# Kernel optimization log

Measured on AMD Instinct MI355X. Metric: run time of the kernel, lower is better.

## Reference

```python
import jax, jax.numpy as jnp
import numpy as np

B = 64; FEAT = 16; T = 32001; BANDS = 8; ND = 16
OUT_LEN = 32000; N_TAPS = 43; K_LATE = 1024
FLIP_PROB = 0.1  # 1 - stickiness (0.9)


def _dense(k, fan_in, fan_out, scale=1.0):
    return jax.random.normal(k, (fan_in, fan_out), jnp.float32) * (scale / np.sqrt(fan_in))


def setup_inputs() -> dict:
    key = jax.random.key(0)
    ks = jax.random.split(key, 20)
    z32 = lambda n: jnp.zeros((n,), jnp.float32)
    inp = {}
    inp['x'] = jax.random.normal(ks[0], (B, FEAT), jnp.float32)
    # stand-in LSTM decoder params: (B, FEAT) -> (B, T, BANDS)
    inp['lstm_W1'] = _dense(ks[1], FEAT, 64); inp['lstm_b1'] = z32(64)
    inp['lstm_W2'] = _dense(ks[2], 64, T * BANDS); inp['lstm_b2'] = z32(T * BANDS)
    # EDCToFDNMapper params
    inp['enc_W1'] = _dense(ks[3], 2 * BANDS, 64); inp['enc_b1'] = z32(64)
    inp['enc_W2'] = _dense(ks[4], 64, 64); inp['enc_b2'] = z32(64)
    inp['del_W1'] = _dense(ks[5], 3 + 64, 64); inp['del_b1'] = z32(64)
    inp['del_W2'] = _dense(ks[6], 64, ND); inp['del_b2'] = z32(ND)
    inp['alp_W1'] = _dense(ks[7], 64, 32); inp['alp_b1'] = z32(32)
    inp['alp_W2'] = _dense(ks[8], 32, ND); inp['alp_b2'] = z32(ND)
    inp['bet_W1'] = _dense(ks[9], 64, 32); inp['bet_b1'] = z32(32)
    inp['bet_W2'] = _dense(ks[10], 32, ND); inp['bet_b2'] = z32(ND)
    # EarlyReflections gains (nn.Parameter, zeros-init in torch; random here to exercise math)
    inp['early_gains'] = jax.random.normal(ks[11], (N_TAPS,), jnp.float32) * 0.1
    # DifferentiableFDN surrogate: causal decaying FIR reverb kernel
    decay = jnp.exp(-jnp.arange(K_LATE, dtype=jnp.float32) / 256.0)
    inp['late_kernel'] = jax.random.normal(ks[12], (K_LATE,), jnp.float32) * 0.05 * decay
    # sticky-sign flip events (constant random draws, flip prob = 1 - stickiness)
    inp['flips'] = (jax.random.uniform(ks[13], (B, OUT_LEN)) < FLIP_PROB).astype(jnp.int32)
    return inp


def _causal_conv(sig, gains):
    # torch: F.conv1d(x[:,None,:], gains.flip(0)[None,None,:], padding=K-1)[:, 0, :L]
    # (torch conv1d is correlation; flipping makes it true convolution with gains)
    K = gains.shape[0]
    y = jax.lax.conv_general_dilated(sig[:, None, :], gains[::-1][None, None, :], (1,),
                                     [(K - 1, K - 1)], dimension_numbers=('NCH', 'OIH', 'NCH'))
    return y[:, 0, :sig.shape[1]]


def _mlp2(h, W1, b1, W2, b2):  # Linear-ReLU-Linear
    return jax.nn.relu(h @ W1 + b1) @ W2 + b2


def reference(x, lstm_W1, lstm_b1, lstm_W2, lstm_b2,
              enc_W1, enc_b1, enc_W2, enc_b2,
              del_W1, del_b1, del_W2, del_b2,
              alp_W1, alp_b1, alp_W2, alp_b2,
              bet_W1, bet_b1, bet_W2, bet_b2,
              early_gains, late_kernel, flips):
    Bx = x.shape[0]
    # LSTM stand-in: (B, FEAT) -> (B, T, BANDS)
    edc_pred = _mlp2(x, lstm_W1, lstm_b1, lstm_W2, lstm_b2).reshape(Bx, T, BANDS)
    edc_1d = edc_pred.mean(axis=2)  # (B, T)
    # EDCToFDNMapper
    edc_mean = edc_pred.mean(axis=1)
    q1 = edc_pred[:, :T // 4, :].mean(axis=1)
    q4 = edc_pred[:, 3 * T // 4:, :].mean(axis=1)
    edc_feat = jnp.concatenate([edc_mean, q4 - q1], axis=1)  # (B, 2*BANDS)
    h = jax.nn.relu(_mlp2(edc_feat, enc_W1, enc_b1, enc_W2, enc_b2))  # Linear-ReLU-Linear-ReLU
    delay_in = jnp.concatenate([x[:, :3], h], axis=1)
    log_kappa = _mlp2(delay_in, del_W1, del_b1, del_W2, del_b2)
    alpha_raw = _mlp2(h, alp_W1, alp_b1, alp_W2, alp_b2)
    beta_raw = _mlp2(h, bet_W1, bet_b1, bet_W2, bet_b2)
    # late reverb (FDN surrogate) + early reflections, both causal convs on edc_1d
    late = _causal_conv(edc_1d, late_kernel)[:, :OUT_LEN]   # (B, 32000)
    early = _causal_conv(edc_1d, early_gains)[:, :OUT_LEN]  # (B, 32000)
    # sign-sticky phase reconstruction: signs = (-1)^cumsum(flips[:,1:]) (parallel parity scan)
    diff = edc_1d[:, :-1] - edc_1d[:, 1:]
    amp = jnp.sqrt(jnp.clip(diff, 0.0))  # (B, T-1) == (B, 32000)
    par = jnp.cumsum(flips.at[:, 0].set(0), axis=1) % 2  # loop starts at t=1; signs[:,0]=+1
    phase = amp * (1.0 - 2.0 * par.astype(amp.dtype))
    rir = (early + late) * phase
    return (rir, edc_pred, log_kappa, alpha_raw, beta_raw)
```

## Files before the change

### kernel.cpp

```cpp
#include <hip/hip_runtime.h>
#include <hip/hip_bf16.h>

#define LJ 256008
#define TN 32001
#define OUT_LEN 32000

typedef __attribute__((ext_vector_type(8))) short short8v;
typedef __attribute__((ext_vector_type(8))) __bf16 bf16x8;
typedef __attribute__((ext_vector_type(4))) float f32x4;

__device__ __forceinline__ unsigned short f2bu(float f) {
    union { __hip_bfloat16 h; unsigned short u; } cv; cv.h = __float2bfloat16(f); return cv.u;
}

__global__ __launch_bounds__(256) void k_h1(const float* __restrict__ x,
                                            const float* __restrict__ W1,
                                            const float* __restrict__ b1,
                                            float* __restrict__ h1)
{
    int idx = blockIdx.x * 256 + threadIdx.x;
    if (idx >= 4096) return;
    int b = idx >> 6, i = idx & 63;
    float acc = b1[i];
    #pragma unroll
    for (int f = 0; f < 16; ++f)
        acc += x[b * 16 + f] * W1[f * 64 + i];
    h1[i * 64 + b] = fmaxf(acc, 0.f);
}

__global__ __launch_bounds__(512, 4) void k_gemm(const float* __restrict__ W2,
                                                 const float* __restrict__ b2,
                                                 const float* __restrict__ h1,
                                                 float* __restrict__ edc,
                                                 float* __restrict__ edc1d,
                                                 float* __restrict__ P)
{
    __shared__ float h1s[4096];
    int tid = threadIdx.x;
    for (int r = tid; r < 4096; r += 512) h1s[r] = h1[r];
    __syncthreads();
    int lane = tid & 63, wv = tid >> 6;
    int bstart = wv * 8;
    long jb4 = (long)blockIdx.x * 256 + 4 * lane;
    bool ok = jb4 < LJ;
    float acc[8][4];
    #pragma unroll
    for (int b = 0; b < 8; ++b)
        #pragma unroll
        for (int c = 0; c < 4; ++c) acc[b][c] = 0.f;
    for (int i = 0; i < 64; ++i) {
        float4 w = ok ? *(const float4*)(W2 + (long)i * LJ + jb4)
                      : make_float4(0.f, 0.f, 0.f, 0.f);
        const float4* hv = (const float4*)(h1s + i * 64 + bstart);
        #pragma unroll
        for (int b4 = 0; b4 < 2; ++b4) {
            float4 h4 = hv[b4];
            acc[b4*4+0][0] += h4.x * w.x; acc[b4*4+0][1] += h4.x * w.y;
            acc[b4*4+0][2] += h4.x * w.z; acc[b4*4+0][3] += h4.x * w.w;
            acc[b4*4+1][0] += h4.y * w.x; acc[b4*4+1][1] += h4.y * w.y;
            acc[b4*4+1][2] += h4.y * w.z; acc[b4*4+1][3] += h4.y * w.w;
            acc[b4*4+2][0] += h4.z * w.x; acc[b4*4+2][1] += h4.z * w.y;
            acc[b4*4+2][2] += h4.z * w.z; acc[b4*4+2][3] += h4.z * w.w;
            acc[b4*4+3][0] += h4.w * w.x; acc[b4*4+3][1] += h4.w * w.y;
            acc[b4*4+3][2] += h4.w * w.z; acc[b4*4+3][3] += h4.w * w.w;
        }
    }
    float4 bias = ok ? *(const float4*)(b2 + jb4) : make_float4(0.f, 0.f, 0.f, 0.f);
    int tcol = (int)(jb4 >> 3);
    #pragma unroll
    for (int b = 0; b < 8; ++b) {
        int bb = bstart + b;
        float r0, r1, r2, r3;
        if (ok) {
            float4 v = make_float4(acc[b][0] + bias.x, acc[b][1] + bias.y,
                                   acc[b][2] + bias.z, acc[b][3] + bias.w);
            *(float4*)(edc + (long)bb * LJ + jb4) = v;
            float s = v.x + v.y + v.z + v.w;
            s += __shfl_xor(s, 1);
            if ((lane & 1) == 0)
                edc1d[(long)bb * TN + tcol] = s * 0.125f;
            r0 = v.x; r1 = v.y; r2 = v.z; r3 = v.w;
        } else { r0 = r1 = r2 = r3 = 0.f; }
        r0 += __shfl_xor(r0, 2);  r1 += __shfl_xor(r1, 2);
        r2 += __shfl_xor(r2, 2);  r3 += __shfl_xor(r3, 2);
        r0 += __shfl_xor(r0, 4);  r1 += __shfl_xor(r1, 4);
        r2 += __shfl_xor(r2, 4);  r3 += __shfl_xor(r3, 4);
        r0 += __shfl_xor(r0, 8);  r1 += __shfl_xor(r1, 8);
        r2 += __shfl_xor(r2, 8);  r3 += __shfl_xor(r3, 8);
        r0 += __shfl_xor(r0, 16); r1 += __shfl_xor(r1, 16);
        r2 += __shfl_xor(r2, 16); r3 += __shfl_xor(r3, 16);
        r0 += __shfl_xor(r0, 32); r1 += __shfl_xor(r1, 32);
        r2 += __shfl_xor(r2, 32); r3 += __shfl_xor(r3, 32);
        if (lane < 2)
            *(float4*)(P + (long)blockIdx.x * 512 + bb * 8 + lane * 4)
                = make_float4(r0, r1, r2, r3);
    }
}

__global__ __launch_bounds__(512) void k_redsum(const float* __restrict__ P,
                                                float* __restrict__ sums)
{
    int g = blockIdx.x, t = threadIdx.x;
    int b = t >> 3, band = t & 7;
    int s0 = g * 16, s1 = s0 + 16;
    if (s1 > 1001) s1 = 1001;
    float all = 0.f, q1 = 0.f, q4 = 0.f;
    for (int blk = s0; blk < s1; ++blk) {
        float v = P[(long)blk * 512 + t];
        all += v;
        if (blk < 250) q1 += v;
        if (blk >= 750) q4 += v;
    }
    atomicAdd(&sums[b * 24 + band * 3 + 0], all);
    atomicAdd(&sums[b * 24 + band * 3 + 1], q1);
    atomicAdd(&sums[b * 24 + band * 3 + 2], q4);
}

__global__ __launch_bounds__(64) void k_mlp(const float* __restrict__ x,
    const float* __restrict__ sums,
    const float* __restrict__ eW1, const float* __restrict__ eb1,
    const float* __restrict__ eW2, const float* __restrict__ eb2,
    const float* __restrict__ dW1, const float* __restrict__ db1,
    const float* __restrict__ dW2, const float* __restrict__ db2,
    const float* __restrict__ aW1, const float* __restrict__ ab1,
    const float* __restrict__ aW2, const float* __restrict__ ab2,
    const float* __restrict__ bW1, const float* __restrict__ bb1,
    const float* __restrict__ bW2, const float* __restrict__ bb2,
    float* __restrict__ out_lk, float* __restrict__ out_a, float* __restrict__ out_b)
{
    int b = blockIdx.x, o = threadIdx.x;
    __shared__ float feat[16], a1[64], hh[64], t1[64];
    if (o < 16) {
        float v;
        if (o < 8) v = sums[b * 24 + o * 3] * (1.f / 32001.f);
        else {
            int band = o - 8;
            v = sums[b * 24 + band * 3 + 2] * (1.f / 8001.f)
              - sums[b * 24 + band * 3 + 1] * (1.f / 8000.f);
        }
        feat[o] = v;
    }
    __syncthreads();
    {   float acc = eb1[o];
        #pragma unroll
        for (int c = 0; c < 16; ++c) acc += feat[c] * eW1[c * 64 + o];
        a1[o] = fmaxf(acc, 0.f); }
    __syncthreads();
    {   float acc = eb2[o];
        for (int c = 0; c < 64; ++c) acc += a1[c] * eW2[c * 64 + o];
        hh[o] = fmaxf(acc, 0.f); }
    __syncthreads();
    {   float acc = db1[o];
        #pragma unroll
        for (int c = 0; c < 3; ++c) acc += x[b * 16 + c] * dW1[c * 64 + o];
        for (int c = 0; c < 64; ++c) acc += hh[c] * dW1[(3 + c) * 64 + o];
        t1[o] = fmaxf(acc, 0.f); }
    __syncthreads();
    if (o < 16) {
        float acc = db2[o];
        for (int c = 0; c < 64; ++c) acc += t1[c] * dW2[c * 16 + o];
        out_lk[b * 16 + o] = acc;
    }
    __syncthreads();
    if (o < 32) {
        float acc = ab1[o];
        for (int c = 0; c < 64; ++c) acc += hh[c] * aW1[c * 32 + o];
        t1[o] = fmaxf(acc, 0.f);
    }
    __syncthreads();
    if (o < 16) {
        float acc = ab2[o];
        for (int c = 0; c < 32; ++c) acc += t1[c] * aW2[c * 16 + o];
        out_a[b * 16 + o] = acc;
    }
    __syncthreads();
    if (o < 32) {
        float acc = bb1[o];
        for (int c = 0; c < 64; ++c) acc += hh[c] * bW1[c * 32 + o];
        t1[o] = fmaxf(acc, 0.f);
    }
    __syncthreads();
    if (o < 16) {
        float acc = bb2[o];
        for (int c = 0; c < 32; ++c) acc += t1[c] * bW2[c * 16 + o];
        out_b[b * 16 + o] = acc;
    }
}

__global__ __launch_bounds__(256) void k_par1(const int* __restrict__ flips,
                                              unsigned* __restrict__ parbits,
                                              unsigned* __restrict__ ctot)
{
    int b = blockIdx.x, c = blockIdx.y, tid = threadIdx.x;
    int t = c * 256 + tid;
    int bit = (t == 0) ? 0 : (flips[(long)b * OUT_LEN + t] & 1);
    int lane = tid & 63, wv = tid >> 6;
    unsigned long long mask = __ballot(bit != 0);
    int below = ((int)__popcll(mask & ((1ull << lane) - 1ull))) & 1;
    int incl = below ^ bit;
    __shared__ int wtot[4];
    if (lane == 0) wtot[wv] = ((int)__popcll(mask)) & 1;
    __syncthreads();
    int pre = 0;
    for (int w = 0; w < wv; ++w) pre ^= wtot[w];
    int inclB = pre ^ incl;
    unsigned long long m2 = __ballot(inclB != 0);
    if (lane == 0)  parbits[b * 1000 + c * 8 + wv * 2 + 0] = (unsigned)(m2 & 0xffffffffull);
    if (lane == 32) parbits[b * 1000 + c * 8 + wv * 2 + 1] = (unsigned)(m2 >> 32);
    if (tid == 0) ctot[c * 64 + b] = (unsigned)(wtot[0] ^ wtot[1] ^ wtot[2] ^ wtot[3]);
}

__global__ __launch_bounds__(64) void k_par2(const unsigned* __restrict__ ctot,
                                             unsigned* __restrict__ cpref)
{
    int b = threadIdx.x;
    unsigned carry = 0;
    for (int c = 0; c < 125; ++c) {
        cpref[c * 64 + b] = carry;
        carry ^= ctot[c * 64 + b];
    }
}

__global__ __launch_bounds__(512) void k_convm(const float* __restrict__ edc1d,
    const float* __restrict__ lk, const float* __restrict__ eg,
    const unsigned* __restrict__ parbits, const unsigned* __restrict__ cpref,
    float* __restrict__ rir)
{
    __shared__ float kerf[1024];
    __shared__ __align__(16) unsigned short afr[33 * 64 * 8];
    __shared__ __align__(16) unsigned short sbf[3136];
    __shared__ float sf32[2049];
    int b = blockIdx.x, tb0 = blockIdx.y * 2048, tid = threadIdx.x;
    const float* src = edc1d + (long)b * TN;
    for (int k = tid; k < 1024; k += 512)
        kerf[k] = lk[k] + (k < 43 ? eg[k] : 0.f);
    for (int ch = tid; ch < 388; ch += 512) {
        unsigned short h[8];
        #pragma unroll
        for (int e = 0; e < 8; ++e) {
            int gt = tb0 + ch * 8 + e - 1031;
            float v = (gt >= 0 && gt <= OUT_LEN) ? src[gt] : 0.f;
            h[e] = f2bu(v);
        }
        int cs = ch ^ ((ch >> 3) & 7);
        *(uint4*)(&sbf[cs * 8]) = make_uint4(
            (unsigned)h[0] | ((unsigned)h[1] << 16), (unsigned)h[2] | ((unsigned)h[3] << 16),
            (unsigned)h[4] | ((unsigned)h[5] << 16), (unsigned)h[6] | ((unsigned)h[7] << 16));
    }
    for (int u = tid; u < 2049; u += 512) {
        int gt = tb0 + u;
        sf32[u] = (gt <= OUT_LEN) ? src[gt] : 0.f;
    }
    __syncthreads();
    for (int sl = tid; sl < 33 * 64; sl += 512) {
        int kb = sl >> 6, l = sl & 63;
        int x0 = kb * 32 - 1 + (l & 15) - 8 * (l >> 4);
        unsigned short h[8];
        #pragma unroll
        for (int e = 0; e < 8; ++e) {
            int x = x0 - e;
            float v = (x >= 0 && x < 1024) ? kerf[x] : 0.f;
            h[e] = f2bu(v);
        }
        *(uint4*)(&afr[sl * 8]) = make_uint4(
            (unsigned)h[0] | ((unsigned)h[1] << 16), (unsigned)h[2] | ((unsigned)h[3] << 16),
            (unsigned)h[4] | ((unsigned)h[5] << 16), (unsigned)h[6] | ((unsigned)h[7] << 16));
    }
    __syncthreads();
    int lane = tid & 63, wv = tid >> 6;
    int tb = tb0 + wv * 256;
    int cq = wv * 256 + 16 * (lane & 15) + 8 * (lane >> 4) + 1032;
    f32x4 acc = {0.f, 0.f, 0.f, 0.f};
    for (int kb = 0; kb < 33; ++kb) {
        short8v araw = *(const short8v*)(&afr[(kb * 64 + lane) * 8]);
        int ch = (cq - (kb << 5)) >> 3;
        int cs = ch ^ ((ch >> 3) & 7);
        short8v braw = *(const short8v*)(&sbf[cs * 8]);
        union { short8v s; bf16x8 v; } ua, ub2;
        ua.s = araw; ub2.s = braw;
        acc = __builtin_amdgcn_mfma_f32_16x16x32_bf16(ua.v, ub2.v, acc, 0, 0, 0);
    }
    int c = lane & 15, q = lane >> 4;
    int t4 = tb + 16 * c + 4 * q;
    if (t4 < OUT_LEN) {
        int u0 = t4 - tb0;
        unsigned pw = parbits[b * 1000 + (t4 >> 5)];
        unsigned cp = cpref[(t4 >> 8) * 64 + b] & 1u;
        int sh = t4 & 31;
        float sv[5];
        #pragma unroll
        for (int e = 0; e < 5; ++e) sv[e] = sf32[u0 + e];
        float r[4];
        #pragma unroll
        for (int reg = 0; reg < 4; ++reg) {
            float diff = sv[reg] - sv[reg + 1];
            float amp = diff > 0.f ? sqrtf(diff) : 0.f;
            unsigned p = ((pw >> (sh + reg)) & 1u) ^ cp;
            r[reg] = acc[reg] * amp * (p ? -1.f : 1.f);
        }
        *(float4*)(rir + (long)b * OUT_LEN + t4) = make_float4(r[0], r[1], r[2], r[3]);
    }
}

extern "C" void kernel_launch(void* const* d_in, const int* in_sizes, int n_in,
                              void* d_out, int out_size, void* d_ws, size_t ws_size,
                              hipStream_t stream) {
    (void)in_sizes; (void)n_in; (void)out_size; (void)ws_size;
    const float* x    = (const float*)d_in[0];
    const float* lW1  = (const float*)d_in[1];  const float* lb1 = (const float*)d_in[2];
    const float* lW2  = (const float*)d_in[3];  const float* lb2 = (const float*)d_in[4];
    const float* eW1  = (const float*)d_in[5];  const float* eb1 = (const float*)d_in[6];
    const float* eW2  = (const float*)d_in[7];  const float* eb2 = (const float*)d_in[8];
    const float* dW1  = (const float*)d_in[9];  const float* db1 = (const float*)d_in[10];
    const float* dW2  = (const float*)d_in[11]; const float* db2 = (const float*)d_in[12];
    const float* aW1  = (const float*)d_in[13]; const float* ab1 = (const float*)d_in[14];
    const float* aW2  = (const float*)d_in[15]; const float* ab2 = (const float*)d_in[16];
    const float* bW1  = (const float*)d_in[17]; const float* bb1 = (const float*)d_in[18];
    const float* bW2  = (const float*)d_in[19]; const float* bb2 = (const float*)d_in[20];
    const float* eg   = (const float*)d_in[21]; const float* lkk = (const float*)d_in[22];
    const int* flips  = (const int*)d_in[23];

    float* out = (float*)d_out;
    float* rir = out;
    float* edc = out + 2048000;
    float* olk = out + 18432512;
    float* oa  = out + 18433536;
    float* ob  = out + 18434560;

    char* wsb = (char*)d_ws;
    float*    ws_h1   = (float*)(wsb + 1024);
    unsigned* ws_ct   = (unsigned*)(wsb + 18432);
    unsigned* ws_cp   = (unsigned*)(wsb + 50688);
    unsigned* ws_pb   = (unsigned*)(wsb + 82944);
    float*    ws_sums = (float*)(wsb + 339200);
    float*    ws_e1d  = (float*)(wsb + 346112);
    float*    ws_part = (float*)(wsb + 8538368);

    hipMemsetAsync(ws_sums, 0, 64 * 24 * sizeof(float), stream);

    k_h1<<<16, 256, 0, stream>>>(x, lW1, lb1, ws_h1);
    k_par1<<<dim3(64, 125), 256, 0, stream>>>(flips, ws_pb, ws_ct);
    k_par2<<<1, 64, 0, stream>>>(ws_ct, ws_cp);
    k_gemm<<<1001, 512, 0, stream>>>(lW2, lb2, ws_h1, edc, ws_e1d, ws_part);
    k_redsum<<<63, 512, 0, stream>>>(ws_part, ws_sums);
    k_mlp<<<64, 64, 0, stream>>>(x, ws_sums, eW1, eb1, eW2, eb2, dW1, db1, dW2, db2,
                                 aW1, ab1, aW2, ab2, bW1, bb1, bW2, bb2, olk, oa, ob);
    k_convm<<<dim3(64, 16), 512, 0, stream>>>(ws_e1d, lkk, eg, ws_pb, ws_cp, rir);
}
```

Before: 105.8 us.

## Stage W2 rows through double-buffered LDS shared across waves in GEMM

Previously each of the 8 waves in a block read the same 64 rows of W2 from global memory, one row per iteration. Now each wave loads one of 8 rows per chunk into a double-buffered shared-memory tile, and all waves read the weights from LDS while the next chunk is prefetched. This aims to cut redundant global/L2 traffic on the large W2 matrix and overlap loads with FMAs. In exchange it adds a barrier per chunk and more LDS use, and it drops the occupancy hint from the launch bounds.

```diff
diff --git a/kernel.cpp b/kernel.cpp
--- a/kernel.cpp
+++ b/kernel.cpp
@@ -28,44 +28,70 @@
     h1[i * 64 + b] = fmaxf(acc, 0.f);
 }
 
-__global__ __launch_bounds__(512, 4) void k_gemm(const float* __restrict__ W2,
-                                                 const float* __restrict__ b2,
-                                                 const float* __restrict__ h1,
-                                                 float* __restrict__ edc,
-                                                 float* __restrict__ edc1d,
-                                                 float* __restrict__ P)
+__global__ __launch_bounds__(512) void k_gemm(const float* __restrict__ W2,
+                                              const float* __restrict__ b2,
+                                              const float* __restrict__ h1,
+                                              float* __restrict__ edc,
+                                              float* __restrict__ edc1d,
+                                              float* __restrict__ P)
 {
     __shared__ float h1s[4096];
+    __shared__ float w2s[2][2048];
     int tid = threadIdx.x;
-    for (int r = tid; r < 4096; r += 512) h1s[r] = h1[r];
-    __syncthreads();
+    #pragma unroll
+    for (int r = 0; r < 8; ++r) h1s[tid + 512 * r] = h1[tid + 512 * r];
     int lane = tid & 63, wv = tid >> 6;
     int bstart = wv * 8;
     long jb4 = (long)blockIdx.x * 256 + 4 * lane;
     bool ok = jb4 < LJ;
+    const float* wb = W2 + (ok ? jb4 : 0);
+    int myslot = wv * 256 + 4 * lane;
     float acc[8][4];
     #pragma unroll
     for (int b = 0; b < 8; ++b)
         #pragma unroll
         for (int c = 0; c < 4; ++c) acc[b][c] = 0.f;
-    for (int i = 0; i < 64; ++i) {
-        float4 w = ok ? *(const float4*)(W2 + (long)i * LJ + jb4)
-                      : make_float4(0.f, 0.f, 0.f, 0.f);
-        const float4* hv = (const float4*)(h1s + i * 64 + bstart);
-        #pragma unroll
-        for (int b4 = 0; b4 < 2; ++b4) {
-            float4 h4 = hv[b4];
-            acc[b4*4+0][0] += h4.x * w.x; acc[b4*4+0][1] += h4.x * w.y;
-            acc[b4*4+0][2] += h4.x * w.z; acc[b4*4+0][3] += h4.x * w.w;
-            acc[b4*4+1][0] += h4.y * w.x; acc[b4*4+1][1] += h4.y * w.y;
-            acc[b4*4+1][2] += h4.y * w.z; acc[b4*4+1][3] += h4.y * w.w;
-            acc[b4*4+2][0] += h4.z * w.x; acc[b4*4+2][1] += h4.z * w.y;
-            acc[b4*4+2][2] += h4.z * w.z; acc[b4*4+2][3] += h4.z * w.w;
-            acc[b4*4+3][0] += h4.w * w.x; acc[b4*4+3][1] += h4.w * w.y;
-            acc[b4*4+3][2] += h4.w * w.z; acc[b4*4+3][3] += h4.w * w.w;
-        }
-    }
-    float4 bias = ok ? *(const float4*)(b2 + jb4) : make_float4(0.f, 0.f, 0.f, 0.f);
+
+    {
+        float4 v0 = *(const float4*)(wb + (long)wv * LJ);
+        *(float4*)(&w2s[0][myslot]) = v0;
+    }
+    __syncthreads();
+
+    #pragma unroll 1
+    for (int cc = 0; cc < 8; ++cc) {
+        int buf = cc & 1;
+        float4 vx;
+        bool more = (cc + 1) < 8;
+        if (more) vx = *(const float4*)(wb + (long)((cc + 1) * 8 + wv) * LJ);
+        #pragma unroll
+        for (int i = 0; i < 8; ++i) {
+            float4 w = *(const float4*)(&w2s[buf][i * 256 + 4 * lane]);
+            const float4* hv = (const float4*)(h1s + (cc * 8 + i) * 64 + bstart);
+            float4 ha = hv[0], hb = hv[1];
+            acc[0][0] += ha.x * w.x; acc[0][1] += ha.x * w.y;
+            acc[0][2] += ha.x * w.z; acc[0][3] += ha.x * w.w;
+            acc[1][0] += ha.y * w.x; acc[1][1] += ha.y * w.y;
+            acc[1][2] += ha.y * w.z; acc[1][3] += ha.y * w.w;
+            acc[2][0] += ha.z * w.x; acc[2][1] += ha.z * w.y;
+            acc[2][2] += ha.z * w.z; acc[2][3] += ha.z * w.w;
+            acc[3][0] += ha.w * w.x; acc[3][1] += ha.w * w.y;
+            acc[3][2] += ha.w * w.z; acc[3][3] += ha.w * w.w;
+            acc[4][0] += hb.x * w.x; acc[4][1] += hb.x * w.y;
+            acc[4][2] += hb.x * w.z; acc[4][3] += hb.x * w.w;
+            acc[5][0] += hb.y * w.x; acc[5][1] += hb.y * w.y;
+            acc[5][2] += hb.y * w.z; acc[5][3] += hb.y * w.w;
+            acc[6][0] += hb.z * w.x; acc[6][1] += hb.z * w.y;
+            acc[6][2] += hb.z * w.z; acc[6][3] += hb.z * w.w;
+            acc[7][0] += hb.w * w.x; acc[7][1] += hb.w * w.y;
+            acc[7][2] += hb.w * w.z; acc[7][3] += hb.w * w.w;
+        }
+        if (more) *(float4*)(&w2s[buf ^ 1][myslot]) = vx;
+        __syncthreads();
+    }
+
+    float4 z4 = make_float4(0.f, 0.f, 0.f, 0.f);
+    float4 bias = ok ? *(const float4*)(b2 + jb4) : z4;
     int tcol = (int)(jb4 >> 3);
     #pragma unroll
     for (int b = 0; b < 8; ++b) {
```

Result: slower. 116.2 us (+9.9%).

## Compute decoder output GEMM with bf16 MFMA and derive band means from band-summed weights

Applied to the files above, without the earlier changes.

Replaces the FP32 FMA outer-product GEMM that produces the decoder output with bf16 16x16x32 MFMA tiles staged through shared memory, in two K halves. The per-time-step band mean is computed separately in FP32 by pre-summing W2 and the bias over each group of eight columns and dotting with h1, so that value keeps full precision. The aim is to cut ALU work in the GEMM. In exchange, the edc output drops to bf16 input precision, and W2 is loaded with narrower strided accesses and read twice.

```diff
diff --git a/kernel.cpp b/kernel.cpp
--- a/kernel.cpp
+++ b/kernel.cpp
@@ -11,6 +11,17 @@
 
 __device__ __forceinline__ unsigned short f2bu(float f) {
     union { __hip_bfloat16 h; unsigned short u; } cv; cv.h = __float2bfloat16(f); return cv.u;
+}
+__device__ __forceinline__ uint4 pack8(const unsigned short* h) {
+    return make_uint4((unsigned)h[0] | ((unsigned)h[1] << 16),
+                      (unsigned)h[2] | ((unsigned)h[3] << 16),
+                      (unsigned)h[4] | ((unsigned)h[5] << 16),
+                      (unsigned)h[6] | ((unsigned)h[7] << 16));
+}
+__device__ __forceinline__ f32x4 mfma16(uint4 a, uint4 b, f32x4 c) {
+    union { uint4 u; short8v s; bf16x8 v; } ua, ub;
+    ua.u = a; ub.u = b;
+    return __builtin_amdgcn_mfma_f32_16x16x32_bf16(ua.v, ub.v, c, 0, 0, 0);
 }
 
 __global__ __launch_bounds__(256) void k_h1(const float* __restrict__ x,
@@ -28,72 +39,158 @@
     h1[i * 64 + b] = fmaxf(acc, 0.f);
 }
 
-__global__ __launch_bounds__(512, 4) void k_gemm(const float* __restrict__ W2,
-                                                 const float* __restrict__ b2,
-                                                 const float* __restrict__ h1,
-                                                 float* __restrict__ edc,
-                                                 float* __restrict__ edc1d,
-                                                 float* __restrict__ P)
-{
-    __shared__ float h1s[4096];
+__global__ __launch_bounds__(512) void k_gemm(const float* __restrict__ W2,
+                                              const float* __restrict__ b2,
+                                              const float* __restrict__ h1,
+                                              float* __restrict__ edc,
+                                              float* __restrict__ edc1d,
+                                              float* __restrict__ P)
+{
+    __shared__ float h1f[4096];
+    __shared__ __align__(16) unsigned short afr[4096];
+    __shared__ __align__(16) unsigned short bfr[8192];
+    __shared__ float wband[2048];
+    __shared__ float bband[32];
     int tid = threadIdx.x;
-    for (int r = tid; r < 4096; r += 512) h1s[r] = h1[r];
-    __syncthreads();
+    long C0 = (long)blockIdx.x * 256;
+
+    #pragma unroll
+    for (int s = 0; s < 8; ++s) h1f[tid + 512 * s] = h1[tid + 512 * s];
+    {
+        int bt = tid >> 7, kb = (tid >> 6) & 1, l = tid & 63;
+        int q = l >> 4, r = l & 15;
+        unsigned short hh[8];
+        #pragma unroll
+        for (int e = 0; e < 8; ++e)
+            hh[e] = f2bu(h1[(32 * kb + 8 * q + e) * 64 + 16 * bt + r]);
+        *(uint4*)(&afr[tid * 8]) = pack8(hh);
+    }
+    #pragma unroll
+    for (int s = 0; s < 4; ++s) {
+        int en = tid + 512 * s;
+        int i = en >> 5, tl = en & 31;
+        long c8 = C0 + 8 * tl;
+        float sum = 0.f;
+        if (c8 + 7 < LJ) {
+            float4 u0 = *(const float4*)(W2 + (long)i * LJ + c8);
+            float4 u1 = *(const float4*)(W2 + (long)i * LJ + c8 + 4);
+            sum = ((u0.x + u0.y) + (u0.z + u0.w)) + ((u1.x + u1.y) + (u1.z + u1.w));
+        }
+        wband[i * 32 + tl] = sum;
+    }
+    if (tid < 32) {
+        long c8 = C0 + 8 * tid;
+        float sum = 0.f;
+        if (c8 + 7 < LJ) {
+            float4 u0 = *(const float4*)(b2 + c8);
+            float4 u1 = *(const float4*)(b2 + c8 + 4);
+            sum = ((u0.x + u0.y) + (u0.z + u0.w)) + ((u1.x + u1.y) + (u1.z + u1.w));
+        }
+        bband[tid] = sum;
+    }
+    #pragma unroll
+    for (int s = 0; s < 2; ++s) {
+        int sl = tid + 512 * s;
+        int ct = sl >> 6, l = sl & 63;
+        int q = l >> 4, r = l & 15;
+        long col = C0 + 16 * ct + r;
+        unsigned short hh[8];
+        #pragma unroll
+        for (int e = 0; e < 8; ++e) {
+            float v = (col < LJ) ? W2[(long)(8 * q + e) * LJ + col] : 0.f;
+            hh[e] = f2bu(v);
+        }
+        *(uint4*)(&bfr[sl * 8]) = pack8(hh);
+    }
+    __syncthreads();
+
     int lane = tid & 63, wv = tid >> 6;
-    int bstart = wv * 8;
-    long jb4 = (long)blockIdx.x * 256 + 4 * lane;
-    bool ok = jb4 < LJ;
-    float acc[8][4];
-    #pragma unroll
-    for (int b = 0; b < 8; ++b)
-        #pragma unroll
-        for (int c = 0; c < 4; ++c) acc[b][c] = 0.f;
-    for (int i = 0; i < 64; ++i) {
-        float4 w = ok ? *(const float4*)(W2 + (long)i * LJ + jb4)
-                      : make_float4(0.f, 0.f, 0.f, 0.f);
-        const float4* hv = (const float4*)(h1s + i * 64 + bstart);
-        #pragma unroll
-        for (int b4 = 0; b4 < 2; ++b4) {
-            float4 h4 = hv[b4];
-            acc[b4*4+0][0] += h4.x * w.x; acc[b4*4+0][1] += h4.x * w.y;
-            acc[b4*4+0][2] += h4.x * w.z; acc[b4*4+0][3] += h4.x * w.w;
-            acc[b4*4+1][0] += h4.y * w.x; acc[b4*4+1][1] += h4.y * w.y;
-            acc[b4*4+1][2] += h4.y * w.z; acc[b4*4+1][3] += h4.y * w.w;
-            acc[b4*4+2][0] += h4.z * w.x; acc[b4*4+2][1] += h4.z * w.y;
-            acc[b4*4+2][2] += h4.z * w.z; acc[b4*4+2][3] += h4.z * w.w;
-            acc[b4*4+3][0] += h4.w * w.x; acc[b4*4+3][1] += h4.w * w.y;
-            acc[b4*4+3][2] += h4.w * w.z; acc[b4*4+3][3] += h4.w * w.w;
-        }
-    }
-    float4 bias = ok ? *(const float4*)(b2 + jb4) : make_float4(0.f, 0.f, 0.f, 0.f);
-    int tcol = (int)(jb4 >> 3);
-    #pragma unroll
-    for (int b = 0; b < 8; ++b) {
-        int bb = bstart + b;
-        float r0, r1, r2, r3;
-        if (ok) {
-            float4 v = make_float4(acc[b][0] + bias.x, acc[b][1] + bias.y,
-                                   acc[b][2] + bias.z, acc[b][3] + bias.w);
-            *(float4*)(edc + (long)bb * LJ + jb4) = v;
-            float s = v.x + v.y + v.z + v.w;
-            s += __shfl_xor(s, 1);
-            if ((lane & 1) == 0)
-                edc1d[(long)bb * TN + tcol] = s * 0.125f;
-            r0 = v.x; r1 = v.y; r2 = v.z; r3 = v.w;
-        } else { r0 = r1 = r2 = r3 = 0.f; }
-        r0 += __shfl_xor(r0, 2);  r1 += __shfl_xor(r1, 2);
-        r2 += __shfl_xor(r2, 2);  r3 += __shfl_xor(r3, 2);
-        r0 += __shfl_xor(r0, 4);  r1 += __shfl_xor(r1, 4);
-        r2 += __shfl_xor(r2, 4);  r3 += __shfl_xor(r3, 4);
-        r0 += __shfl_xor(r0, 8);  r1 += __shfl_xor(r1, 8);
-        r2 += __shfl_xor(r2, 8);  r3 += __shfl_xor(r3, 8);
-        r0 += __shfl_xor(r0, 16); r1 += __shfl_xor(r1, 16);
-        r2 += __shfl_xor(r2, 16); r3 += __shfl_xor(r3, 16);
-        r0 += __shfl_xor(r0, 32); r1 += __shfl_xor(r1, 32);
-        r2 += __shfl_xor(r2, 32); r3 += __shfl_xor(r3, 32);
-        if (lane < 2)
-            *(float4*)(P + (long)blockIdx.x * 512 + bb * 8 + lane * 4)
-                = make_float4(r0, r1, r2, r3);
+    int q = lane >> 4, r = lane & 15;
+    f32x4 acc[2][4];
+    #pragma unroll
+    for (int c = 0; c < 2; ++c)
+        #pragma unroll
+        for (int b = 0; b < 4; ++b) acc[c][b] = (f32x4){0.f, 0.f, 0.f, 0.f};
+
+    #pragma unroll
+    for (int ctl = 0; ctl < 2; ++ctl) {
+        int ct = wv * 2 + ctl;
+        uint4 braw = *(const uint4*)(&bfr[(ct * 64 + lane) * 8]);
+        #pragma unroll
+        for (int bt = 0; bt < 4; ++bt) {
+            uint4 araw = *(const uint4*)(&afr[((bt * 2 + 0) * 64 + lane) * 8]);
+            acc[ctl][bt] = mfma16(araw, braw, acc[ctl][bt]);
+        }
+    }
+    __syncthreads();
+    #pragma unroll
+    for (int s = 0; s < 2; ++s) {
+        int sl = tid + 512 * s;
+        int ct = sl >> 6, l = sl & 63;
+        int qq = l >> 4, rr = l & 15;
+        long col = C0 + 16 * ct + rr;
+        unsigned short hh[8];
+        #pragma unroll
+        for (int e = 0; e < 8; ++e) {
+            float v = (col < LJ) ? W2[(long)(32 + 8 * qq + e) * LJ + col] : 0.f;
+            hh[e] = f2bu(v);
+        }
+        *(uint4*)(&bfr[sl * 8]) = pack8(hh);
+    }
+    __syncthreads();
+    #pragma unroll
+    for (int ctl = 0; ctl < 2; ++ctl) {
+        int ct = wv * 2 + ctl;
+        uint4 braw = *(const uint4*)(&bfr[(ct * 64 + lane) * 8]);
+        #pragma unroll
+        for (int bt = 0; bt < 4; ++bt) {
+            uint4 araw = *(const uint4*)(&afr[((bt * 2 + 1) * 64 + lane) * 8]);
+            acc[ctl][bt] = mfma16(araw, braw, acc[ctl][bt]);
+        }
+    }
+
+    #pragma unroll
+    for (int s = 0; s < 4; ++s) {
+        int en = tid + 512 * s;
+        int b = en >> 5, tl = en & 31;
+        long c8 = C0 + 8 * tl;
+        if (c8 + 7 < LJ) {
+            float dot = bband[tl];
+            #pragma unroll 8
+            for (int i = 0; i < 64; ++i)
+                dot += h1f[i * 64 + b] * wband[i * 32 + tl];
+            edc1d[(long)b * TN + (C0 >> 3) + tl] = dot * 0.125f;
+        }
+    }
+
+    float psum[4][4];
+    #pragma unroll
+    for (int bt = 0; bt < 4; ++bt)
+        #pragma unroll
+        for (int rg = 0; rg < 4; ++rg) psum[bt][rg] = 0.f;
+    #pragma unroll
+    for (int ctl = 0; ctl < 2; ++ctl) {
+        int ct = wv * 2 + ctl;
+        long col = C0 + 16 * ct + r;
+        bool okc = col < LJ;
+        float bias = okc ? b2[col] : 0.f;
+        #pragma unroll
+        for (int bt = 0; bt < 4; ++bt) {
+            #pragma unroll
+            for (int rg = 0; rg < 4; ++rg) {
+                float v = acc[ctl][bt][rg] + bias;
+                if (okc) edc[(long)(16 * bt + 4 * q + rg) * LJ + col] = v;
+                float sps = v + __shfl_xor(v, 8);
+                psum[bt][rg] += sps;
+            }
+        }
+    }
+    if (r < 8) {
+        #pragma unroll
+        for (int bt = 0; bt < 4; ++bt)
+            #pragma unroll
+            for (int rg = 0; rg < 4; ++rg)
+                P[(long)blockIdx.x * 512 + (16 * bt + 4 * q + rg) * 8 + r] = psum[bt][rg];
     }
 }
 
@@ -243,9 +340,7 @@
             h[e] = f2bu(v);
         }
         int cs = ch ^ ((ch >> 3) & 7);
-        *(uint4*)(&sbf[cs * 8]) = make_uint4(
-            (unsigned)h[0] | ((unsigned)h[1] << 16), (unsigned)h[2] | ((unsigned)h[3] << 16),
-            (unsigned)h[4] | ((unsigned)h[5] << 16), (unsigned)h[6] | ((unsigned)h[7] << 16));
+        *(uint4*)(&sbf[cs * 8]) = pack8(h);
     }
     for (int u = tid; u < 2049; u += 512) {
         int gt = tb0 + u;
@@ -262,9 +357,7 @@
             float v = (x >= 0 && x < 1024) ? kerf[x] : 0.f;
             h[e] = f2bu(v);
         }
-        *(uint4*)(&afr[sl * 8]) = make_uint4(
-            (unsigned)h[0] | ((unsigned)h[1] << 16), (unsigned)h[2] | ((unsigned)h[3] << 16),
-            (unsigned)h[4] | ((unsigned)h[5] << 16), (unsigned)h[6] | ((unsigned)h[7] << 16));
+        *(uint4*)(&afr[sl * 8]) = pack8(h);
     }
     __syncthreads();
     int lane = tid & 63, wv = tid >> 6;
@@ -272,13 +365,11 @@
     int cq = wv * 256 + 16 * (lane & 15) + 8 * (lane >> 4) + 1032;
     f32x4 acc = {0.f, 0.f, 0.f, 0.f};
     for (int kb = 0; kb < 33; ++kb) {
-        short8v araw = *(const short8v*)(&afr[(kb * 64 + lane) * 8]);
+        uint4 araw = *(const uint4*)(&afr[(kb * 64 + lane) * 8]);
         int ch = (cq - (kb << 5)) >> 3;
         int cs = ch ^ ((ch >> 3) & 7);
-        short8v braw = *(const short8v*)(&sbf[cs * 8]);
-        union { short8v s; bf16x8 v; } ua, ub2;
-        ua.s = araw; ub2.s = braw;
-        acc = __builtin_amdgcn_mfma_f32_16x16x32_bf16(ua.v, ub2.v, acc, 0, 0, 0);
+        uint4 braw = *(const uint4*)(&sbf[cs * 8]);
+        acc = mfma16(araw, braw, acc);
     }
     int c = lane & 15, q = lane >> 4;
     int t4 = tb + 16 * c + 4 * q;
```

New measurement: 116.0 us. 9.6% more time.
